# Performance work log

Measured on AMD Instinct MI355X. Metric: run time of the kernel, lower is better.

## Reference

```python
import jax, jax.numpy as jnp
import numpy as np

N_NODES = 100000
N_EDGES = 1600000
IN_CH = 64
HID = 64
OUT = 2


def sage_conv(x, src, dst, W_agg, W_root, b):
    # PyG SAGEConv (mean aggr): out = lin_l(mean_{j in N(i)} x_j) + lin_r(x_i)
    n = x.shape[0]
    msgs = x[src]                                        # [E, F] gather
    agg = jax.ops.segment_sum(msgs, dst, num_segments=n)  # [N, F] scatter-add
    cnt = jax.ops.segment_sum(jnp.ones((src.shape[0], 1), x.dtype), dst, num_segments=n)
    agg = agg / jnp.maximum(cnt, 1)                      # mean; isolated nodes -> 0
    return agg @ W_agg + x @ W_root + b


def setup_inputs() -> dict:
    key = jax.random.key(0)
    ks = jax.random.split(key, 8)
    s = lambda f: 1.0 / np.sqrt(f)
    x = jax.random.normal(ks[0], (N_NODES, IN_CH), dtype=jnp.float32)
    edge_index = jax.random.randint(ks[1], (2, N_EDGES), 0, N_NODES, dtype=jnp.int64)
    return {
        "x": x,
        "edge_index": edge_index,
        "W1_agg": jax.random.normal(ks[2], (IN_CH, HID), dtype=jnp.float32) * s(IN_CH),
        "W1_root": jax.random.normal(ks[3], (IN_CH, HID), dtype=jnp.float32) * s(IN_CH),
        "b1": jnp.zeros((HID,), jnp.float32),
        "W2_agg": jax.random.normal(ks[4], (HID, HID), dtype=jnp.float32) * s(HID),
        "W2_root": jax.random.normal(ks[5], (HID, HID), dtype=jnp.float32) * s(HID),
        "b2": jnp.zeros((HID,), jnp.float32),
        "W_lin": jax.random.normal(ks[6], (HID, OUT), dtype=jnp.float32) * s(HID),
        "b_lin": jnp.zeros((OUT,), jnp.float32),
    }


def reference(x, edge_index, W1_agg, W1_root, b1, W2_agg, W2_root, b2, W_lin, b_lin):
    src, dst = edge_index[0], edge_index[1]
    h = jax.nn.relu(sage_conv(x, src, dst, W1_agg, W1_root, b1))   # dropout = identity (eval)
    h = jax.nn.relu(sage_conv(h, src, dst, W2_agg, W2_root, b2))
    return h @ W_lin + b_lin
```

## Files before the change

### kernel.cpp

```cpp
#include <hip/hip_runtime.h>
#include <hip/hip_bf16.h>

#define FEAT 64
#define CHUNK 8192
#define MAX_NB 1024

typedef __attribute__((ext_vector_type(8))) short bf16x8;
typedef __attribute__((ext_vector_type(4))) float f32x4;
typedef __attribute__((ext_vector_type(2))) float f32x2;

__device__ __forceinline__ float bflo2f(unsigned int u) {
    union { unsigned int u; float f; } v; v.u = u << 16; return v.f;
}
__device__ __forceinline__ float bfhi2f(unsigned int u) {
    union { unsigned int u; float f; } v; v.u = u & 0xffff0000u; return v.f;
}
__device__ __forceinline__ unsigned short f2bf(float f) {
    union { float f; unsigned int u; } v; v.f = f;
    unsigned int u = v.u;
    u += 0x7fffu + ((u >> 16) & 1u);
    return (unsigned short)(u >> 16);
}
__device__ __forceinline__ f32x2 bfpair(unsigned int u) {
    f32x2 r; r.x = bflo2f(u & 0xffffu); r.y = bfhi2f(u); return r;
}

__global__ void detect_kernel(const unsigned short* __restrict__ xh,
                              const int* __restrict__ ei32,
                              int* __restrict__ flags) {
    __shared__ int cnt_bf, cnt_nz;
    int tid = threadIdx.x;
    if (tid == 0) { cnt_bf = 0; cnt_nz = 0; }
    __syncthreads();
    unsigned short h = xh[tid * 2];
    int e = (h >> 7) & 0xFF;
    if (e >= 110 && e <= 132) atomicAdd(&cnt_bf, 1);
    if (ei32[tid * 2 + 1] != 0) atomicAdd(&cnt_nz, 1);
    __syncthreads();
    if (tid == 0) {
        flags[0] = (cnt_bf >= 128) ? 1 : 0;
        flags[1] = (cnt_nz < 8) ? 1 : 0;
    }
}

__global__ void cvt_x_kernel(const void* __restrict__ in, unsigned short* __restrict__ out16,
                             int n8, const int* __restrict__ flags) {
    if (flags[0]) return;
    int i = blockIdx.x * 256 + threadIdx.x;
    if (i >= n8) return;
    float4 a = ((const float4*)in)[2 * i];
    float4 b = ((const float4*)in)[2 * i + 1];
    uint4 o;
    o.x = (unsigned int)f2bf(a.x) | ((unsigned int)f2bf(a.y) << 16);
    o.y = (unsigned int)f2bf(a.z) | ((unsigned int)f2bf(a.w) << 16);
    o.z = (unsigned int)f2bf(b.x) | ((unsigned int)f2bf(b.y) << 16);
    o.w = (unsigned int)f2bf(b.z) | ((unsigned int)f2bf(b.w) << 16);
    ((uint4*)out16)[i] = o;
}

__global__ void cvt_weights_kernel(const void* __restrict__ w1a, const void* __restrict__ w1r,
                                   const void* __restrict__ b1,  const void* __restrict__ w2a,
                                   const void* __restrict__ w2r, const void* __restrict__ b2,
                                   const void* __restrict__ wl,  const void* __restrict__ bl,
                                   float* __restrict__ out, unsigned short* __restrict__ Wt,
                                   const int* __restrict__ flags) {
    int i = blockIdx.x * 256 + threadIdx.x;
    if (i >= 16642) return;
    const void* src; int off;
    if      (i < 4096)  { src = w1a; off = i; }
    else if (i < 8192)  { src = w1r; off = i - 4096; }
    else if (i < 8256)  { src = b1;  off = i - 8192; }
    else if (i < 12352) { src = w2a; off = i - 8256; }
    else if (i < 16448) { src = w2r; off = i - 12352; }
    else if (i < 16512) { src = b2;  off = i - 16448; }
    else if (i < 16640) { src = wl;  off = i - 16512; }
    else                { src = bl;  off = i - 16640; }
    float v = flags[0] ? bflo2f(((const unsigned short*)src)[off])
                       : ((const float*)src)[off];
    out[i] = v;
    unsigned short hv = f2bf(v);
    if (i < 4096)                      Wt[(off & 63) * 128 + (off >> 6)] = hv;
    else if (i < 8192)                 Wt[(off & 63) * 128 + 64 + (off >> 6)] = hv;
    else if (i >= 8256 && i < 12352)   Wt[8192 + (off & 63) * 128 + (off >> 6)] = hv;
    else if (i >= 12352 && i < 16448)  Wt[8192 + (off & 63) * 128 + 64 + (off >> 6)] = hv;
}

__global__ __launch_bounds__(256) void p1_hist_kernel(
    const int* __restrict__ ei32, int* __restrict__ hist,
    int E, int N, int NB, int EC, const int* __restrict__ flags) {
    __shared__ int lh[MAX_NB];
    int tid = threadIdx.x, c = blockIdx.x;
    for (int i = tid; i < NB; i += 256) lh[i] = 0;
    __syncthreads();
    int idx64 = flags[1];
    long base = (long)c * CHUNK;
#pragma unroll 4
    for (int j = 0; j < CHUNK / 256; ++j) {
        long e = base + j * 256 + tid;
        if (e < E) {
            int d = idx64 ? ei32[2 * ((long)E + e)] : ei32[(long)E + e];
            if ((unsigned)d < (unsigned)N)
                atomicAdd(&lh[d >> 8], 1);
        }
    }
    __syncthreads();
    for (int k = tid; k < NB; k += 256) hist[(long)k * EC + c] = lh[k];
}

__global__ __launch_bounds__(256) void scan1_kernel(const int* __restrict__ in,
                                                    int* __restrict__ out,
                                                    int* __restrict__ blocksum, int n) {
    int tid = threadIdx.x;
    int base = blockIdx.x * 2048 + tid * 8;
    int v[8];
    int tsum = 0;
#pragma unroll
    for (int i = 0; i < 8; ++i) {
        v[i] = (base + i < n) ? in[base + i] : 0;
        tsum += v[i];
    }
    int lane = tid & 63;
    int x = tsum;
#pragma unroll
    for (int off = 1; off < 64; off <<= 1) {
        int y = __shfl_up(x, off);
        if (lane >= off) x += y;
    }
    __shared__ int wsum[4];
    int wave = tid >> 6;
    if (lane == 63) wsum[wave] = x;
    __syncthreads();
    int woff = 0;
#pragma unroll
    for (int w = 0; w < 4; ++w) if (w < wave) woff += wsum[w];
    int run = woff + x - tsum;
#pragma unroll
    for (int i = 0; i < 8; ++i) {
        if (base + i < n) out[base + i] = run;
        run += v[i];
    }
    if (tid == 255) blocksum[blockIdx.x] = woff + x;
}

__global__ void scan3_kernel(int* __restrict__ out, const int* __restrict__ blocksum, int n) {
    int i = blockIdx.x * 256 + threadIdx.x;
    if (i >= n) return;
    int nb = i >> 11;
    int pre = 0;
    for (int b = 0; b < nb; ++b) pre += blocksum[b];
    out[i] += pre;
}

__global__ __launch_bounds__(256) void p3_scatter_kernel(
    const int* __restrict__ ei32, const int* __restrict__ hscan,
    int* __restrict__ bkt, int E, int N, int NB, int EC,
    const int* __restrict__ flags) {
    __shared__ int lh[MAX_NB];
    int tid = threadIdx.x, c = blockIdx.x;
    for (int i = tid; i < NB; i += 256) lh[i] = 0;
    __syncthreads();
    int idx64 = flags[1];
    long base = (long)c * CHUNK;
#pragma unroll 4
    for (int j = 0; j < CHUNK / 256; ++j) {
        long e = base + j * 256 + tid;
        if (e < E) {
            int s = idx64 ? ei32[2 * e]             : ei32[e];
            int d = idx64 ? ei32[2 * ((long)E + e)] : ei32[(long)E + e];
            if ((unsigned)d < (unsigned)N) {
                if ((unsigned)s >= (unsigned)N) s = 0;
                int k = d >> 8;
                int r = atomicAdd(&lh[k], 1);
                bkt[hscan[(long)k * EC + c] + r] = s | ((d & 255) << 20);
            }
        }
    }
}

__global__ __launch_bounds__(256) void p4_build_kernel(
    const int* __restrict__ bkt, const int* __restrict__ hscan, const int* __restrict__ hist,
    int* __restrict__ offs, int* __restrict__ cnt, int* __restrict__ srcs,
    int E, int N, int NB, int EC) {
    int k = blockIdx.x, tid = threadIdx.x;
    int start = hscan[(long)k * EC];
    int end = (k + 1 < NB) ? hscan[(long)(k + 1) * EC]
                           : (hscan[(long)NB * EC - 1] + hist[(long)NB * EC - 1]);
    __shared__ int lc[256], lheads[256], wsum[4];
    lc[tid] = 0;
    __syncthreads();
    for (int e = start + tid; e < end; e += 256)
        atomicAdd(&lc[(bkt[e] >> 20) & 255], 1);
    __syncthreads();
    int cv = lc[tid];
    int lane = tid & 63, wave = tid >> 6;
    int x = cv;
#pragma unroll
    for (int off = 1; off < 64; off <<= 1) {
        int y = __shfl_up(x, off);
        if (lane >= off) x += y;
    }
    if (lane == 63) wsum[wave] = x;
    __syncthreads();
    int woff = 0;
#pragma unroll
    for (int w = 0; w < 4; ++w) if (w < wave) woff += wsum[w];
    int excl = woff + x - cv;
    int gnode = k * 256 + tid;
    if (gnode < N) { offs[gnode] = start + excl; cnt[gnode] = cv; }
    lheads[tid] = excl;
    __syncthreads();
    for (int e = start + tid; e < end; e += 256) {
        int p = bkt[e];
        int d8 = (p >> 20) & 255;
        int pos = start + atomicAdd(&lheads[d8], 1);
        srcs[pos] = p & 0xFFFFF;
    }
}

__global__ __launch_bounds__(256) void aggregate_kernel(
    const void* __restrict__ feat_raw, const unsigned short* __restrict__ feat_ws,
    const int* __restrict__ srcs,
    const int* __restrict__ offs, const int* __restrict__ cnt,
    unsigned short* __restrict__ agg16, int N, const int* __restrict__ flags) {
    const unsigned short* feat16 = flags[0] ? (const unsigned short*)feat_raw : feat_ws;
    long gid = (long)blockIdx.x * 256 + threadIdx.x;
    int node = (int)(gid >> 6);
    if (node >= N) return;
    int lane = threadIdx.x & 63;
    int g = lane >> 3;
    int li = lane & 7;
    int start = offs[node];
    int deg = cnt[node];
    int end = start + deg;
    f32x2 a0 = {0.f, 0.f}, a1 = a0, a2 = a0, a3 = a0;
    int e = start;
    for (; e + 16 <= end; e += 16) {
        int s0 = srcs[e + g];
        int s1 = srcs[e + 8 + g];
        uint4 u0 = *(const uint4*)(feat16 + (size_t)s0 * FEAT + 8 * li);
        uint4 u1 = *(const uint4*)(feat16 + (size_t)s1 * FEAT + 8 * li);
        a0 += bfpair(u0.x); a1 += bfpair(u0.y); a2 += bfpair(u0.z); a3 += bfpair(u0.w);
        a0 += bfpair(u1.x); a1 += bfpair(u1.y); a2 += bfpair(u1.z); a3 += bfpair(u1.w);
    }
    for (; e < end; e += 8) {
        int idx = e + g;
        bool ok = idx < end;
        int s = srcs[ok ? idx : end - 1];
        uint4 u = *(const uint4*)(feat16 + (size_t)s * FEAT + 8 * li);
        if (ok) {
            a0 += bfpair(u.x); a1 += bfpair(u.y); a2 += bfpair(u.z); a3 += bfpair(u.w);
        }
    }
    float acc[8] = {a0.x, a0.y, a1.x, a1.y, a2.x, a2.y, a3.x, a3.y};
#pragma unroll
    for (int i = 0; i < 8; ++i) {
        acc[i] += __shfl_xor(acc[i], 8);
        acc[i] += __shfl_xor(acc[i], 16);
        acc[i] += __shfl_xor(acc[i], 32);
    }
    if (g == 0) {
        float inv = 1.0f / (float)(deg > 0 ? deg : 1);
        uint4 o;
        o.x = (unsigned)f2bf(acc[0] * inv) | ((unsigned)f2bf(acc[1] * inv) << 16);
        o.y = (unsigned)f2bf(acc[2] * inv) | ((unsigned)f2bf(acc[3] * inv) << 16);
        o.z = (unsigned)f2bf(acc[4] * inv) | ((unsigned)f2bf(acc[5] * inv) << 16);
        o.w = (unsigned)f2bf(acc[6] * inv) | ((unsigned)f2bf(acc[7] * inv) << 16);
        *(uint4*)(agg16 + (size_t)node * FEAT + 8 * li) = o;
    }
}

__global__ __launch_bounds__(256) void sage_gemm_kernel(
    const unsigned short* __restrict__ agg16,
    const void* __restrict__ root_raw, const unsigned short* __restrict__ root_ws,
    const unsigned short* __restrict__ Wt, const float* __restrict__ bias,
    unsigned short* __restrict__ out16, int N,
    const float* __restrict__ wl, const float* __restrict__ bl,
    void* __restrict__ out_final, const int* __restrict__ flags, int root_sel) {

    const unsigned short* root16 =
        (root_sel && !flags[0]) ? root_ws : (const unsigned short*)root_raw;

    __shared__ unsigned short A_l[64][136];
    __shared__ unsigned short B_l[64][136];

    int tid = threadIdx.x;
    int blk = blockIdx.x;

#pragma unroll
    for (int i = 0; i < 4; ++i) {
        int ch = tid + i * 256;
        int n = ch >> 4, kc = ch & 15;
        *(uint4*)&B_l[n][kc * 8] = *(const uint4*)(Wt + n * 128 + kc * 8);
    }
#pragma unroll
    for (int i = 0; i < 4; ++i) {
        int ch = tid + i * 256;
        int r = ch >> 4, c = ch & 15;
        int row = blk * 64 + r;
        uint4 u = make_uint4(0, 0, 0, 0);
        if (row < N)
            u = (c < 8) ? ((const uint4*)(agg16 + (size_t)row * FEAT))[c]
                        : ((const uint4*)(root16 + (size_t)row * FEAT))[c - 8];
        *(uint4*)&A_l[r][c * 8] = u;
    }
    __syncthreads();

    int lane = tid & 63;
    int wave = tid >> 6;
    int r0 = wave * 16;
    int m = lane & 15, quad = lane >> 4;

    f32x4 acc0 = {0.f, 0.f, 0.f, 0.f};
    f32x4 acc1 = acc0, acc2 = acc0, acc3 = acc0;

#pragma unroll
    for (int k0 = 0; k0 < 128; k0 += 32) {
        bf16x8 a = *(const bf16x8*)&A_l[r0 + m][k0 + quad * 8];
        bf16x8 b0 = *(const bf16x8*)&B_l[ 0 + m][k0 + quad * 8];
        bf16x8 b1 = *(const bf16x8*)&B_l[16 + m][k0 + quad * 8];
        bf16x8 b2 = *(const bf16x8*)&B_l[32 + m][k0 + quad * 8];
        bf16x8 b3 = *(const bf16x8*)&B_l[48 + m][k0 + quad * 8];
        acc0 = __builtin_amdgcn_mfma_f32_16x16x32_bf16(a, b0, acc0, 0, 0, 0);
        acc1 = __builtin_amdgcn_mfma_f32_16x16x32_bf16(a, b1, acc1, 0, 0, 0);
        acc2 = __builtin_amdgcn_mfma_f32_16x16x32_bf16(a, b2, acc2, 0, 0, 0);
        acc3 = __builtin_amdgcn_mfma_f32_16x16x32_bf16(a, b3, acc3, 0, 0, 0);
    }
    __syncthreads();

#pragma unroll
    for (int c = 0; c < 4; ++c) {
        f32x4 av = (c == 0) ? acc0 : (c == 1) ? acc1 : (c == 2) ? acc2 : acc3;
        float bv = bias[c * 16 + m];
#pragma unroll
        for (int reg = 0; reg < 4; ++reg) {
            float v = fmaxf(av[reg] + bv, 0.f);
            A_l[r0 + quad * 4 + reg][c * 16 + m] = f2bf(v);
        }
    }
    __syncthreads();

#pragma unroll
    for (int i = 0; i < 2; ++i) {
        int ch = tid + i * 256;
        int r = ch >> 3, c = ch & 7;
        int row = blk * 64 + r;
        if (row < N)
            ((uint4*)(out16 + (size_t)row * FEAT))[c] = *(const uint4*)&A_l[r][c * 8];
    }

    if (wl) {
        int r = tid >> 2, part = tid & 3;
        int row = blk * 64 + r;
        if (row < N) {
            float p0 = 0.f, p1 = 0.f;
#pragma unroll
            for (int j = 0; j < 16; ++j) {
                int f = part * 16 + j;
                float v = bflo2f(A_l[r][f]);
                p0 += v * wl[f * 2 + 0];
                p1 += v * wl[f * 2 + 1];
            }
            p0 += __shfl_down(p0, 2, 4); p0 += __shfl_down(p0, 1, 4);
            p1 += __shfl_down(p1, 2, 4); p1 += __shfl_down(p1, 1, 4);
            if (part == 0) {
                p0 += bl[0];
                p1 += bl[1];
                if (flags[0]) {
                    unsigned int o = ((unsigned int)f2bf(p1) << 16) | (unsigned int)f2bf(p0);
                    ((unsigned int*)out_final)[row] = o;
                } else {
                    ((float2*)out_final)[row] = make_float2(p0, p1);
                }
            }
        }
    }
}

extern "C" void kernel_launch(void* const* d_in, const int* in_sizes, int n_in,
                              void* d_out, int out_size, void* d_ws, size_t ws_size,
                              hipStream_t stream) {
    const void* x_in = d_in[0];
    const int*  ei32 = (const int*)d_in[1];

    int N = in_sizes[0] / FEAT;
    int E = in_sizes[1] / 2;
    int NB = (N + 255) >> 8;
    int EC = (E + CHUNK - 1) / CHUNK;
    int HN = NB * EC;

    unsigned short* x16   = (unsigned short*)d_ws;
    unsigned short* h16   = x16 + (size_t)N * FEAT;
    unsigned short* agg16 = h16 + (size_t)N * FEAT;
    unsigned short* Wt    = agg16 + (size_t)N * FEAT;
    float*          wbuf  = (float*)(Wt + 16384);
    int*            hist  = (int*)(wbuf + 16704);
    int*            hscan = hist + HN;
    int*            bsum  = hscan + HN;
    int*            flags = bsum + 1024;
    int*            offs  = flags + 16;
    int*            cnt   = offs + N;
    int*            bkt   = cnt + N;
    int*            srcs  = bkt + E;

    float* b1_32 = wbuf + 8192;
    float* b2_32 = wbuf + 16448;
    float* wl32  = wbuf + 16512;
    float* bl32  = wbuf + 16640;

    detect_kernel<<<1, 256, 0, stream>>>((const unsigned short*)x_in, ei32, flags);

    int n8 = N * FEAT / 8;
    cvt_x_kernel<<<(n8 + 255) / 256, 256, 0, stream>>>(x_in, x16, n8, flags);
    cvt_weights_kernel<<<(16642 + 255) / 256, 256, 0, stream>>>(
        d_in[2], d_in[3], d_in[4], d_in[5], d_in[6], d_in[7], d_in[8], d_in[9],
        wbuf, Wt, flags);

    p1_hist_kernel<<<EC, 256, 0, stream>>>(ei32, hist, E, N, NB, EC, flags);
    int sB = (HN + 2047) / 2048;
    scan1_kernel<<<sB, 256, 0, stream>>>(hist, hscan, bsum, HN);
    scan3_kernel<<<(HN + 255) / 256, 256, 0, stream>>>(hscan, bsum, HN);
    p3_scatter_kernel<<<EC, 256, 0, stream>>>(ei32, hscan, bkt, E, N, NB, EC, flags);
    p4_build_kernel<<<NB, 256, 0, stream>>>(bkt, hscan, hist, offs, cnt, srcs, E, N, NB, EC);

    int aBlocks = (int)(((long)N * 64 + 255) / 256);
    int gBlocks = (N + 63) / 64;

    aggregate_kernel<<<aBlocks, 256, 0, stream>>>(x_in, x16, srcs, offs, cnt, agg16, N, flags);
    sage_gemm_kernel<<<gBlocks, 256, 0, stream>>>(agg16, x_in, x16, Wt, b1_32, h16, N,
                                                  nullptr, nullptr, nullptr, flags, 1);

    aggregate_kernel<<<aBlocks, 256, 0, stream>>>(h16, h16, srcs, offs, cnt, agg16, N, flags);
    sage_gemm_kernel<<<gBlocks, 256, 0, stream>>>(agg16, h16, h16, Wt + 8192, b2_32, h16, N,
                                                  wl32, bl32, d_out, flags, 0);
}
```

Measured before the change: 254.6 us.

## Fuse detect and conversion kernels; map aggregation to 8 lanes per node

Merges the format-detection, x conversion and weight conversion launches into one prep kernel, in which every block recomputes the detection flags locally, removing two kernel launches. The aggregation kernel now assigns 8 lanes per node (8 nodes per wave) instead of a whole 64-lane wave per node. Each group loops serially over its node's neighbours with a 4-way unroll, which removes the cross-lane shuffle reduction. This raises node-level parallelism and memory-level parallelism for the mean-degree-16 graph, but each group reads the neighbour indices serially and high-degree nodes can cause divergence within a wave.

```diff
diff --git a/kernel.cpp b/kernel.cpp
--- a/kernel.cpp
+++ b/kernel.cpp
@@ -25,9 +25,15 @@
     f32x2 r; r.x = bflo2f(u & 0xffffu); r.y = bfhi2f(u); return r;
 }
 
-__global__ void detect_kernel(const unsigned short* __restrict__ xh,
-                              const int* __restrict__ ei32,
-                              int* __restrict__ flags) {
+__global__ __launch_bounds__(256) void prep_kernel(
+    const unsigned short* __restrict__ xh, const int* __restrict__ ei32,
+    const void* __restrict__ w1a, const void* __restrict__ w1r,
+    const void* __restrict__ b1,  const void* __restrict__ w2a,
+    const void* __restrict__ w2r, const void* __restrict__ b2,
+    const void* __restrict__ wl,  const void* __restrict__ bl,
+    float* __restrict__ wbuf, unsigned short* __restrict__ Wt,
+    int* __restrict__ flags, const void* __restrict__ x_in,
+    unsigned short* __restrict__ x16, int n8) {
     __shared__ int cnt_bf, cnt_nz;
     int tid = threadIdx.x;
     if (tid == 0) { cnt_bf = 0; cnt_nz = 0; }
@@ -37,52 +43,41 @@
     if (e >= 110 && e <= 132) atomicAdd(&cnt_bf, 1);
     if (ei32[tid * 2 + 1] != 0) atomicAdd(&cnt_nz, 1);
     __syncthreads();
-    if (tid == 0) {
-        flags[0] = (cnt_bf >= 128) ? 1 : 0;
+    int f0 = (cnt_bf >= 128) ? 1 : 0;
+    if (blockIdx.x == 0 && tid == 0) {
+        flags[0] = f0;
         flags[1] = (cnt_nz < 8) ? 1 : 0;
     }
-}
-
-__global__ void cvt_x_kernel(const void* __restrict__ in, unsigned short* __restrict__ out16,
-                             int n8, const int* __restrict__ flags) {
-    if (flags[0]) return;
-    int i = blockIdx.x * 256 + threadIdx.x;
-    if (i >= n8) return;
-    float4 a = ((const float4*)in)[2 * i];
-    float4 b = ((const float4*)in)[2 * i + 1];
-    uint4 o;
-    o.x = (unsigned int)f2bf(a.x) | ((unsigned int)f2bf(a.y) << 16);
-    o.y = (unsigned int)f2bf(a.z) | ((unsigned int)f2bf(a.w) << 16);
-    o.z = (unsigned int)f2bf(b.x) | ((unsigned int)f2bf(b.y) << 16);
-    o.w = (unsigned int)f2bf(b.z) | ((unsigned int)f2bf(b.w) << 16);
-    ((uint4*)out16)[i] = o;
-}
-
-__global__ void cvt_weights_kernel(const void* __restrict__ w1a, const void* __restrict__ w1r,
-                                   const void* __restrict__ b1,  const void* __restrict__ w2a,
-                                   const void* __restrict__ w2r, const void* __restrict__ b2,
-                                   const void* __restrict__ wl,  const void* __restrict__ bl,
-                                   float* __restrict__ out, unsigned short* __restrict__ Wt,
-                                   const int* __restrict__ flags) {
-    int i = blockIdx.x * 256 + threadIdx.x;
-    if (i >= 16642) return;
-    const void* src; int off;
-    if      (i < 4096)  { src = w1a; off = i; }
-    else if (i < 8192)  { src = w1r; off = i - 4096; }
-    else if (i < 8256)  { src = b1;  off = i - 8192; }
-    else if (i < 12352) { src = w2a; off = i - 8256; }
-    else if (i < 16448) { src = w2r; off = i - 12352; }
-    else if (i < 16512) { src = b2;  off = i - 16448; }
-    else if (i < 16640) { src = wl;  off = i - 16512; }
-    else                { src = bl;  off = i - 16640; }
-    float v = flags[0] ? bflo2f(((const unsigned short*)src)[off])
-                       : ((const float*)src)[off];
-    out[i] = v;
-    unsigned short hv = f2bf(v);
-    if (i < 4096)                      Wt[(off & 63) * 128 + (off >> 6)] = hv;
-    else if (i < 8192)                 Wt[(off & 63) * 128 + 64 + (off >> 6)] = hv;
-    else if (i >= 8256 && i < 12352)   Wt[8192 + (off & 63) * 128 + (off >> 6)] = hv;
-    else if (i >= 12352 && i < 16448)  Wt[8192 + (off & 63) * 128 + 64 + (off >> 6)] = hv;
+    int i = blockIdx.x * 256 + tid;
+    if (i < 16642) {
+        const void* src; int off;
+        if      (i < 4096)  { src = w1a; off = i; }
+        else if (i < 8192)  { src = w1r; off = i - 4096; }
+        else if (i < 8256)  { src = b1;  off = i - 8192; }
+        else if (i < 12352) { src = w2a; off = i - 8256; }
+        else if (i < 16448) { src = w2r; off = i - 12352; }
+        else if (i < 16512) { src = b2;  off = i - 16448; }
+        else if (i < 16640) { src = wl;  off = i - 16512; }
+        else                { src = bl;  off = i - 16640; }
+        float v = f0 ? bflo2f(((const unsigned short*)src)[off])
+                     : ((const float*)src)[off];
+        wbuf[i] = v;
+        unsigned short hv = f2bf(v);
+        if (i < 4096)                      Wt[(off & 63) * 128 + (off >> 6)] = hv;
+        else if (i < 8192)                 Wt[(off & 63) * 128 + 64 + (off >> 6)] = hv;
+        else if (i >= 8256 && i < 12352)   Wt[8192 + (off & 63) * 128 + (off >> 6)] = hv;
+        else if (i >= 12352 && i < 16448)  Wt[8192 + (off & 63) * 128 + 64 + (off >> 6)] = hv;
+    }
+    if (!f0 && i < n8) {
+        float4 a = ((const float4*)x_in)[2 * i];
+        float4 b = ((const float4*)x_in)[2 * i + 1];
+        uint4 o;
+        o.x = (unsigned int)f2bf(a.x) | ((unsigned int)f2bf(a.y) << 16);
+        o.y = (unsigned int)f2bf(a.z) | ((unsigned int)f2bf(a.w) << 16);
+        o.z = (unsigned int)f2bf(b.x) | ((unsigned int)f2bf(b.y) << 16);
+        o.w = (unsigned int)f2bf(b.z) | ((unsigned int)f2bf(b.w) << 16);
+        ((uint4*)x16)[i] = o;
+    }
 }
 
 __global__ __launch_bounds__(256) void p1_hist_kernel(
@@ -223,50 +218,43 @@
     const int* __restrict__ offs, const int* __restrict__ cnt,
     unsigned short* __restrict__ agg16, int N, const int* __restrict__ flags) {
     const unsigned short* feat16 = flags[0] ? (const unsigned short*)feat_raw : feat_ws;
-    long gid = (long)blockIdx.x * 256 + threadIdx.x;
-    int node = (int)(gid >> 6);
-    if (node >= N) return;
-    int lane = threadIdx.x & 63;
+    int tid = threadIdx.x;
+    int lane = tid & 63;
+    int wave = tid >> 6;
     int g = lane >> 3;
     int li = lane & 7;
+    int node = (blockIdx.x * 4 + wave) * 8 + g;
+    if (node >= N) return;
     int start = offs[node];
     int deg = cnt[node];
-    int end = start + deg;
     f32x2 a0 = {0.f, 0.f}, a1 = a0, a2 = a0, a3 = a0;
-    int e = start;
-    for (; e + 16 <= end; e += 16) {
-        int s0 = srcs[e + g];
-        int s1 = srcs[e + 8 + g];
+    int j = 0;
+    for (; j + 4 <= deg; j += 4) {
+        int s0 = srcs[start + j];
+        int s1 = srcs[start + j + 1];
+        int s2 = srcs[start + j + 2];
+        int s3 = srcs[start + j + 3];
         uint4 u0 = *(const uint4*)(feat16 + (size_t)s0 * FEAT + 8 * li);
         uint4 u1 = *(const uint4*)(feat16 + (size_t)s1 * FEAT + 8 * li);
+        uint4 u2 = *(const uint4*)(feat16 + (size_t)s2 * FEAT + 8 * li);
+        uint4 u3 = *(const uint4*)(feat16 + (size_t)s3 * FEAT + 8 * li);
         a0 += bfpair(u0.x); a1 += bfpair(u0.y); a2 += bfpair(u0.z); a3 += bfpair(u0.w);
         a0 += bfpair(u1.x); a1 += bfpair(u1.y); a2 += bfpair(u1.z); a3 += bfpair(u1.w);
-    }
-    for (; e < end; e += 8) {
-        int idx = e + g;
-        bool ok = idx < end;
-        int s = srcs[ok ? idx : end - 1];
+        a0 += bfpair(u2.x); a1 += bfpair(u2.y); a2 += bfpair(u2.z); a3 += bfpair(u2.w);
+        a0 += bfpair(u3.x); a1 += bfpair(u3.y); a2 += bfpair(u3.z); a3 += bfpair(u3.w);
+    }
+    for (; j < deg; ++j) {
+        int s = srcs[start + j];
         uint4 u = *(const uint4*)(feat16 + (size_t)s * FEAT + 8 * li);
-        if (ok) {
-            a0 += bfpair(u.x); a1 += bfpair(u.y); a2 += bfpair(u.z); a3 += bfpair(u.w);
-        }
-    }
-    float acc[8] = {a0.x, a0.y, a1.x, a1.y, a2.x, a2.y, a3.x, a3.y};
-#pragma unroll
-    for (int i = 0; i < 8; ++i) {
-        acc[i] += __shfl_xor(acc[i], 8);
-        acc[i] += __shfl_xor(acc[i], 16);
-        acc[i] += __shfl_xor(acc[i], 32);
-    }
-    if (g == 0) {
-        float inv = 1.0f / (float)(deg > 0 ? deg : 1);
-        uint4 o;
-        o.x = (unsigned)f2bf(acc[0] * inv) | ((unsigned)f2bf(acc[1] * inv) << 16);
-        o.y = (unsigned)f2bf(acc[2] * inv) | ((unsigned)f2bf(acc[3] * inv) << 16);
-        o.z = (unsigned)f2bf(acc[4] * inv) | ((unsigned)f2bf(acc[5] * inv) << 16);
-        o.w = (unsigned)f2bf(acc[6] * inv) | ((unsigned)f2bf(acc[7] * inv) << 16);
-        *(uint4*)(agg16 + (size_t)node * FEAT + 8 * li) = o;
-    }
+        a0 += bfpair(u.x); a1 += bfpair(u.y); a2 += bfpair(u.z); a3 += bfpair(u.w);
+    }
+    float inv = 1.0f / (float)(deg > 0 ? deg : 1);
+    uint4 o;
+    o.x = (unsigned)f2bf(a0.x * inv) | ((unsigned)f2bf(a0.y * inv) << 16);
+    o.y = (unsigned)f2bf(a1.x * inv) | ((unsigned)f2bf(a1.y * inv) << 16);
+    o.z = (unsigned)f2bf(a2.x * inv) | ((unsigned)f2bf(a2.y * inv) << 16);
+    o.w = (unsigned)f2bf(a3.x * inv) | ((unsigned)f2bf(a3.y * inv) << 16);
+    *(uint4*)(agg16 + (size_t)node * FEAT + 8 * li) = o;
 }
 
 __global__ __launch_bounds__(256) void sage_gemm_kernel(
@@ -407,13 +395,13 @@
     float* wl32  = wbuf + 16512;
     float* bl32  = wbuf + 16640;
 
-    detect_kernel<<<1, 256, 0, stream>>>((const unsigned short*)x_in, ei32, flags);
-
     int n8 = N * FEAT / 8;
-    cvt_x_kernel<<<(n8 + 255) / 256, 256, 0, stream>>>(x_in, x16, n8, flags);
-    cvt_weights_kernel<<<(16642 + 255) / 256, 256, 0, stream>>>(
+    int pBlocks = (n8 + 255) / 256;
+    if (pBlocks < 66) pBlocks = 66;
+    prep_kernel<<<pBlocks, 256, 0, stream>>>(
+        (const unsigned short*)x_in, ei32,
         d_in[2], d_in[3], d_in[4], d_in[5], d_in[6], d_in[7], d_in[8], d_in[9],
-        wbuf, Wt, flags);
+        wbuf, Wt, flags, x_in, x16, n8);
 
     p1_hist_kernel<<<EC, 256, 0, stream>>>(ei32, hist, E, N, NB, EC, flags);
     int sB = (HN + 2047) / 2048;
@@ -422,7 +410,7 @@
     p3_scatter_kernel<<<EC, 256, 0, stream>>>(ei32, hscan, bkt, E, N, NB, EC, flags);
     p4_build_kernel<<<NB, 256, 0, stream>>>(bkt, hscan, hist, offs, cnt, srcs, E, N, NB, EC);
 
-    int aBlocks = (int)(((long)N * 64 + 255) / 256);
+    int aBlocks = (N + 31) / 32;
     int gBlocks = (N + 63) / 64;
 
     aggregate_kernel<<<aBlocks, 256, 0, stream>>>(x_in, x16, srcs, offs, cnt, agg16, N, flags);
```

Result: faster. 236.2 us (-7.2%).
